# Performance work log

Hardware: AMD Instinct MI355X
Metric: run time of the kernel (lower is better)

## Reference

```python
import jax, jax.numpy as jnp
import numpy as np

N = 50000       # nodes
E = 800000      # edges (avg degree 16)
C_IN = 128
C_OUT = 64
C_HID = 2 * C_OUT  # 128, per Dir_Encoder_GCN


def gcn_conv(x, W, b, src, dst, ew, n):
    """PyG GCNConv: add self-loops (weight 1), symmetric normalization,
    aggregate transformed source features at destination, add bias."""
    loops = jnp.arange(n)
    s = jnp.concatenate([src, loops])                       # [E+N]
    d = jnp.concatenate([dst, loops])                       # [E+N]
    w = jnp.concatenate([ew, jnp.ones((n,), ew.dtype)])     # [E+N]
    deg = jax.ops.segment_sum(w, d, num_segments=n)         # weighted in-degree
    dinv = jnp.where(deg > 0, jax.lax.rsqrt(deg), 0.0)      # deg^{-1/2}
    norm = dinv[s] * w * dinv[d]                            # [E+N]
    xw = x @ W                                              # [n, out]
    out = jax.ops.segment_sum(xw[s] * norm[:, None], d, num_segments=n)
    return out + b


def setup_inputs() -> dict:
    key = jax.random.key(0)
    k1, k2, k3, k4, k5, k6, k7 = jax.random.split(key, 7)
    x = jax.random.normal(k1, (N, C_IN), dtype=jnp.float32)
    edge_index = jax.random.randint(k2, (2, E), 0, N, dtype=jnp.int64)
    edge_weight = jax.random.uniform(k3, (E,), dtype=jnp.float32)
    W1 = jax.random.normal(k4, (C_IN, C_HID), dtype=jnp.float32) * (1.0 / np.sqrt(C_IN))
    b1 = jnp.zeros((C_HID,), dtype=jnp.float32)
    W2 = jax.random.normal(k5, (C_HID, C_OUT), dtype=jnp.float32) * (1.0 / np.sqrt(C_HID))
    b2 = jnp.zeros((C_OUT,), dtype=jnp.float32)
    return {"x": x, "edge_index": edge_index, "edge_weight": edge_weight,
            "W1": W1, "b1": b1, "W2": W2, "b2": b2}


def reference(x, edge_index, edge_weight, W1, b1, W2, b2):
    src, dst = edge_index[0], edge_index[1]
    n = x.shape[0]
    h = jax.nn.elu(gcn_conv(x, W1, b1, src, dst, edge_weight, n))
    return jax.nn.softplus(gcn_conv(h, W2, b2, src, dst, edge_weight, n)) + 1e-4
```

## Files before the change

### kernel.cpp

```cpp
#include <hip/hip_runtime.h>
#include <math.h>

constexpr int CAP    = 48;
constexpr int CAPP   = 49;
constexpr int BIN    = 128;
constexpr int SEGCAP = 2432;
constexpr int CE     = 3136;

typedef short v8s __attribute__((ext_vector_type(8)));
typedef float v4f __attribute__((ext_vector_type(4)));


__device__ __forceinline__ uint f2bf(float f) {
    union { float f; uint i; } v; v.f = f;
    uint r = v.i + 0x7FFFu + ((v.i >> 16) & 1u);
    return r >> 16;
}
__device__ __forceinline__ float bf2f(uint h) {
    union { uint i; float f; } v; v.i = h << 16;
    return v.f;
}
__device__ __forceinline__ void bf8_expand(uint4 q, float* o) {
    uint u[4] = {q.x, q.y, q.z, q.w};
#pragma unroll
    for (int j = 0; j < 4; ++j) {
        union { uint i; float f; } lo, hi;
        lo.i = u[j] << 16;
        hi.i = u[j] & 0xFFFF0000u;
        o[2 * j] = lo.f;
        o[2 * j + 1] = hi.f;
    }
}


template <int COLS>
__device__ __forceinline__ void pack_one(const float* __restrict__ W,
                                         ushort* __restrict__ wpk, int id) {
    constexpr int NT = COLS / 16;
    int lane = id & 63;
    int t = (id >> 6) % NT;
    int c = (id >> 6) / NT;
    int ncol = t * 16 + (lane & 15);
    int k0 = c * 32 + (lane >> 4) * 8;
    ushort hi[8], lo[8];
#pragma unroll
    for (int j = 0; j < 8; ++j) {
        float v = W[(size_t)(k0 + j) * COLS + ncol];
        ushort h = (ushort)f2bf(v);
        hi[j] = h;
        lo[j] = (ushort)f2bf(v - bf2f(h));
    }
    size_t bh = ((size_t)(c * NT + t) * 64 + lane) * 8;
    size_t bl = ((size_t)((4 + c) * NT + t) * 64 + lane) * 8;
    *(uint4*)(wpk + bh) = *(uint4*)hi;
    *(uint4*)(wpk + bl) = *(uint4*)lo;
}

__global__ __launch_bounds__(256) void k_prep(const float* __restrict__ W1,
                                              const float* __restrict__ W2,
                                              ushort* __restrict__ wpk1,
                                              ushort* __restrict__ wpk2,
                                              int* __restrict__ g_bin_cnt) {
    const int blk = blockIdx.x;
    const int tid = threadIdx.x;
    if (blk == 0) {
        g_bin_cnt[tid] = 0;
        g_bin_cnt[tid + 256] = 0;
        return;
    }
    int id = (blk - 1) * 256 + tid;
    if (id < 2048) pack_one<128>(W1, wpk1, id);
    else if (id < 3072) pack_one<64>(W2, wpk2, id - 2048);
}


__global__ __launch_bounds__(256) void k_p1(const int* __restrict__ src,
                                            const int* __restrict__ dst,
                                            const float* __restrict__ ew,
                                            int* __restrict__ g_bin_cnt,
                                            int2* __restrict__ seg, int E) {
    __shared__ int hist[512];
    __shared__ int base[512];
    const int tid = threadIdx.x;
    const int e0 = blockIdx.x * CE;
    const int e1 = min(e0 + CE, E);

    hist[tid] = 0;
    hist[tid + 256] = 0;
    __syncthreads();
    for (int e = e0 + tid; e < e1; e += 256) atomicAdd(&hist[dst[e] >> 7], 1);
    __syncthreads();
    for (int b = tid; b < 512; b += 256)
        base[b] = (hist[b] > 0) ? atomicAdd(&g_bin_cnt[b], hist[b]) : 0;
    __syncthreads();
    hist[tid] = 0;
    hist[tid + 256] = 0;
    __syncthreads();
    for (int e = e0 + tid; e < e1; e += 256) {
        int d = dst[e];
        int b = d >> 7;
        int r = atomicAdd(&hist[b], 1);
        int slot = base[b] + r;
        if (slot < SEGCAP)
            seg[(size_t)b * SEGCAP + slot] =
                make_int2(((d & 127) << 16) | src[e], __float_as_int(ew[e]));
    }
}


__global__ __launch_bounds__(256) void k_p2(const int* __restrict__ g_bin_cnt,
                                            const int2* __restrict__ seg,
                                            int* __restrict__ cnt, float* __restrict__ dinv,
                                            uint* __restrict__ bucket, int N) {
    __shared__ uint lb[BIN * CAPP];
    __shared__ int lcnt[BIN];
    __shared__ float ldeg[BIN];
    const int b = blockIdx.x;
    const int tid = threadIdx.x;
    if (tid < BIN) { lcnt[tid] = 0; ldeg[tid] = 0.f; }
    __syncthreads();

    const int m = min(g_bin_cnt[b], SEGCAP);
    const int2* s = seg + (size_t)b * SEGCAP;
    for (int i = tid; i < m; i += 256) {
        int2 p = s[i];
        int dl = (p.x >> 16) & 127;
        uint sv = (uint)(p.x & 0xFFFF);
        float w = __int_as_float(p.y);
        int slot = atomicAdd(&lcnt[dl], 1);
        if (slot < CAP) lb[dl * CAPP + slot] = sv | (f2bf(w) << 16);
        atomicAdd(&ldeg[dl], w);
    }
    __syncthreads();

    const int node0 = b * BIN;
    if (tid < BIN && node0 + tid < N) {
        cnt[node0 + tid] = min(lcnt[tid], CAP);
        dinv[node0 + tid] = rsqrtf(1.0f + ldeg[tid]);
    }
    const int nn = min(BIN, N - node0);
    for (int i = tid; i < nn * CAP; i += 256) {
        int nl = i / CAP;
        int j = i - nl * CAP;
        if (j < min(lcnt[nl], CAP))
            bucket[((size_t)node0 + nl) * CAP + j] = lb[nl * CAPP + j];
    }
}


__global__ __launch_bounds__(256) void k_gemm1(const float* __restrict__ X,
                                               const ushort* __restrict__ wpk,
                                               const float* __restrict__ dinv,
                                               ushort* __restrict__ Y, int n) {
    constexpr int NT = 8;
    const int wave = threadIdx.x >> 6;
    const int lane = threadIdx.x & 63;
    const int m = lane & 15;
    const int q = lane >> 4;
    const int r0 = blockIdx.x * 64 + wave * 16;

    v4f acc[NT];
#pragma unroll
    for (int t = 0; t < NT; ++t) acc[t] = (v4f){0.f, 0.f, 0.f, 0.f};

    const int arow = min(r0 + m, n - 1);

    for (int c = 0; c < 4; ++c) {
        const float* xp = X + (size_t)arow * 128 + c * 32 + q * 8;
        float4 v0 = *(const float4*)xp;
        float4 v1 = *(const float4*)(xp + 4);
        float f[8] = {v0.x, v0.y, v0.z, v0.w, v1.x, v1.y, v1.z, v1.w};
        union { ushort u[8]; v8s v; } H, L;
#pragma unroll
        for (int j = 0; j < 8; ++j) {
            ushort h = (ushort)f2bf(f[j]);
            H.u[j] = h;
            L.u[j] = (ushort)f2bf(f[j] - bf2f(h));
        }
#pragma unroll
        for (int t = 0; t < NT; ++t) {
            v8s b_hi = *(const v8s*)(wpk + ((size_t)(c * NT + t) * 64 + lane) * 8);
            v8s b_lo = *(const v8s*)(wpk + ((size_t)((4 + c) * NT + t) * 64 + lane) * 8);
            acc[t] = __builtin_amdgcn_mfma_f32_16x16x32_bf16(H.v, b_hi, acc[t], 0, 0, 0);
            acc[t] = __builtin_amdgcn_mfma_f32_16x16x32_bf16(H.v, b_lo, acc[t], 0, 0, 0);
            acc[t] = __builtin_amdgcn_mfma_f32_16x16x32_bf16(L.v, b_hi, acc[t], 0, 0, 0);
        }
    }

#pragma unroll
    for (int r = 0; r < 4; ++r) {
        int row = r0 + q * 4 + r;
        if (row < n) {
            float sc = dinv[row];
#pragma unroll
            for (int t = 0; t < NT; ++t)
                Y[(size_t)row * 128 + t * 16 + m] = (ushort)f2bf(acc[t][r] * sc);
        }
    }
}


template <int C>
__device__ __forceinline__ void gather_accum(const ushort* __restrict__ xw,
                                             const uint* __restrict__ bk, int c,
                                             int laneoff, float* acc) {
    int i = 0;
    for (; i + 8 <= c; i += 8) {
        uint4 e0 = *(const uint4*)(bk + i);
        uint4 e1 = *(const uint4*)(bk + i + 4);
        uint ee[8] = {e0.x, e0.y, e0.z, e0.w, e1.x, e1.y, e1.z, e1.w};
        uint4 q[8];
#pragma unroll
        for (int u = 0; u < 8; ++u)
            q[u] = *(const uint4*)(xw + (size_t)(ee[u] & 0xFFFF) * C + laneoff);
#pragma unroll
        for (int u = 0; u < 8; ++u) {
            float w = bf2f(ee[u] >> 16);
            float f[8];
            bf8_expand(q[u], f);
#pragma unroll
            for (int j = 0; j < 8; ++j) acc[j] += f[j] * w;
        }
    }
    for (; i + 4 <= c; i += 4) {
        uint4 e0 = *(const uint4*)(bk + i);
        uint ee[4] = {e0.x, e0.y, e0.z, e0.w};
        uint4 q[4];
#pragma unroll
        for (int u = 0; u < 4; ++u)
            q[u] = *(const uint4*)(xw + (size_t)(ee[u] & 0xFFFF) * C + laneoff);
#pragma unroll
        for (int u = 0; u < 4; ++u) {
            float w = bf2f(ee[u] >> 16);
            float f[8];
            bf8_expand(q[u], f);
#pragma unroll
            for (int j = 0; j < 8; ++j) acc[j] += f[j] * w;
        }
    }
    for (; i < c; ++i) {
        uint e = bk[i];
        float w = bf2f(e >> 16);
        uint4 qq = *(const uint4*)(xw + (size_t)(e & 0xFFFF) * C + laneoff);
        float f[8];
        bf8_expand(qq, f);
#pragma unroll
        for (int j = 0; j < 8; ++j) acc[j] += f[j] * w;
    }
}


__global__ __launch_bounds__(256) void k_gather_g2(const ushort* __restrict__ xw,
                                                   const float* __restrict__ dinv,
                                                   const float* __restrict__ b1,
                                                   const int* __restrict__ cnt,
                                                   const uint* __restrict__ bucket,
                                                   const ushort* __restrict__ wpk2,
                                                   ushort* __restrict__ hw, int n) {
    constexpr int HS = 136;
    __shared__ ushort hrow[16 * HS];
    __shared__ float sdd[16];
    const int tid = threadIdx.x;
    const int node_l = tid >> 4;
    const int lane16 = tid & 15;
    const int node0 = blockIdx.x * 16;
    const int node = node0 + node_l;
    const bool active = node < n;

    float acc[8] = {0.f, 0.f, 0.f, 0.f, 0.f, 0.f, 0.f, 0.f};
    if (active) {
        {
            float sf[8];
            uint4 q = *(const uint4*)(xw + (size_t)node * 128 + lane16 * 8);
            bf8_expand(q, sf);
#pragma unroll
            for (int j = 0; j < 8; ++j) acc[j] = sf[j];
        }
        int c = min(cnt[node], CAP);
        gather_accum<128>(xw, bucket + (size_t)node * CAP, c, lane16 * 8, acc);

        float dd = dinv[node];
        if (lane16 == 0) sdd[node_l] = dd;
        float4 b0 = *(const float4*)(b1 + lane16 * 8);
        float4 bv = *(const float4*)(b1 + lane16 * 8 + 4);
        float bb[8] = {b0.x, b0.y, b0.z, b0.w, bv.x, bv.y, bv.z, bv.w};
#pragma unroll
        for (int j = 0; j < 8; ++j) {
            float v = bb[j] + dd * acc[j];
            acc[j] = v > 0.f ? v : expm1f(v);
        }
    } else {
        if (lane16 == 0) sdd[node_l] = 0.f;
#pragma unroll
        for (int j = 0; j < 8; ++j) acc[j] = 0.f;
    }

    uint4 o;
    o.x = f2bf(acc[0]) | (f2bf(acc[1]) << 16);
    o.y = f2bf(acc[2]) | (f2bf(acc[3]) << 16);
    o.z = f2bf(acc[4]) | (f2bf(acc[5]) << 16);
    o.w = f2bf(acc[6]) | (f2bf(acc[7]) << 16);
    *(uint4*)(hrow + node_l * HS + lane16 * 8) = o;
    __syncthreads();

    const int wave = tid >> 6;
    const int lane = tid & 63;
    const int mm = lane & 15;
    const int qq = lane >> 4;
    v4f c4 = (v4f){0.f, 0.f, 0.f, 0.f};
    for (int c = 0; c < 4; ++c) {
        v8s a = *(const v8s*)(hrow + mm * HS + c * 32 + qq * 8);
        v8s b_hi = *(const v8s*)(wpk2 + ((size_t)(c * 4 + wave) * 64 + lane) * 8);
        v8s b_lo = *(const v8s*)(wpk2 + ((size_t)((4 + c) * 4 + wave) * 64 + lane) * 8);
        c4 = __builtin_amdgcn_mfma_f32_16x16x32_bf16(a, b_hi, c4, 0, 0, 0);
        c4 = __builtin_amdgcn_mfma_f32_16x16x32_bf16(a, b_lo, c4, 0, 0, 0);
    }
#pragma unroll
    for (int r = 0; r < 4; ++r) {
        int nl = qq * 4 + r;
        int row = node0 + nl;
        if (row < n)
            hw[(size_t)row * 64 + wave * 16 + mm] = (ushort)f2bf(c4[r] * sdd[nl]);
    }
}


__global__ __launch_bounds__(256) void k_gather2(const ushort* __restrict__ hw,
                                                 const float* __restrict__ dinv,
                                                 const float* __restrict__ b2,
                                                 const int* __restrict__ cnt,
                                                 const uint* __restrict__ bucket,
                                                 float* __restrict__ out, int n) {
    constexpr int C = 64, L = 8;
    int node = blockIdx.x * 32 + threadIdx.x / L;
    int lane = threadIdx.x % L;
    if (node >= n) return;

    float acc[8];
    {
        float sf[8];
        uint4 q = *(const uint4*)(hw + (size_t)node * C + lane * 8);
        bf8_expand(q, sf);
#pragma unroll
        for (int j = 0; j < 8; ++j) acc[j] = sf[j];
    }

    int c = min(cnt[node], CAP);
    gather_accum<64>(hw, bucket + (size_t)node * CAP, c, lane * 8, acc);

    float dd = dinv[node];
    float4 b0 = *(const float4*)(b2 + lane * 8);
    float4 bv = *(const float4*)(b2 + lane * 8 + 4);
    float bb[8] = {b0.x, b0.y, b0.z, b0.w, bv.x, bv.y, bv.z, bv.w};
#pragma unroll
    for (int j = 0; j < 8; ++j) {
        float v = bb[j] + dd * acc[j];
        acc[j] = ((v > 20.f) ? v : log1pf(expf(v))) + 1e-4f;
    }
    *(float4*)(out + (size_t)node * C + lane * 8) =
        make_float4(acc[0], acc[1], acc[2], acc[3]);
    *(float4*)(out + (size_t)node * C + lane * 8 + 4) =
        make_float4(acc[4], acc[5], acc[6], acc[7]);
}


extern "C" void kernel_launch(void* const* d_in, const int* in_sizes, int n_in,
                              void* d_out, int out_size, void* d_ws, size_t ws_size,
                              hipStream_t stream) {
    const float* x  = (const float*)d_in[0];
    const int*   ei = (const int*)d_in[1];
    const float* ew = (const float*)d_in[2];
    const float* W1 = (const float*)d_in[3];
    const float* b1 = (const float*)d_in[4];
    const float* W2 = (const float*)d_in[5];
    const float* b2 = (const float*)d_in[6];

    const int N = in_sizes[0] / 128;
    const int E = in_sizes[1] / 2;
    const int* src = ei;
    const int* dst = ei + E;
    float* y = (float*)d_out;

    const int nbins = (N + BIN - 1) / BIN;

    char* p = (char*)d_ws;
    auto take = [&](size_t bytes) {
        char* q = p;
        p += (bytes + 255) & ~(size_t)255;
        return q;
    };

    int*    g_bin_cnt = (int*)take(512 * 4);
    int2*   seg       = (int2*)take((size_t)nbins * SEGCAP * 8);
    int*    cnt       = (int*)take((size_t)N * 4);
    float*  dinv      = (float*)take((size_t)N * 4);
    uint*   bucket    = (uint*)take((size_t)N * CAP * 4);
    ushort* xw        = (ushort*)take((size_t)N * 128 * 2);
    ushort* hw        = (ushort*)take((size_t)N * 64 * 2);
    ushort* wpk1      = (ushort*)take(2 * 4 * 8 * 64 * 8 * 2);
    ushort* wpk2      = (ushort*)take(2 * 4 * 4 * 64 * 8 * 2);

    auto cdiv = [](int a, int b) { return (a + b - 1) / b; };

    k_prep<<<13, 256, 0, stream>>>(W1, W2, wpk1, wpk2, g_bin_cnt);
    k_p1<<<cdiv(E, CE), 256, 0, stream>>>(src, dst, ew, g_bin_cnt, seg, E);
    k_p2<<<nbins, 256, 0, stream>>>(g_bin_cnt, seg, cnt, dinv, bucket, N);

    k_gemm1<<<cdiv(N, 64), 256, 0, stream>>>(x, wpk1, dinv, xw, N);
    k_gather_g2<<<cdiv(N, 16), 256, 0, stream>>>(xw, dinv, b1, cnt, bucket, wpk2, hw, N);
    k_gather2<<<cdiv(N, 32), 256, 0, stream>>>(hw, dinv, b2, cnt, bucket, y, N);
}
```

Before: 192.2 us.

## Co-schedule GEMM1 with edge binning and apply source dinv in gather

Merges the first feature GEMM and the edge-binning pass into one launch whose blocks branch by index, so the compute-bound GEMM can overlap the memory-bound histogram/scatter. To make that possible, the source-side dinv scaling is moved out of the GEMM epilogue and into the gathers, which now load dinv per neighbour. Binning now does a per-block local prefix sum into shared memory with coalesced write-out and per-block offsets, removing the global atomic counter and its zeroing. k_p2 then reads each bin's slice from every block's segment. The costs are an extra scattered dinv load per edge and k_p2 doing 256 short strided reads per bin. k_p2 indexes offsets by thread id, which assumes at most 256 binning blocks (true for this E).

```diff
diff --git a/kernel.cpp b/kernel.cpp
--- a/kernel.cpp
+++ b/kernel.cpp
@@ -1,11 +1,11 @@
 #include <hip/hip_runtime.h>
 #include <math.h>
 
-constexpr int CAP    = 48;
-constexpr int CAPP   = 49;
-constexpr int BIN    = 128;
-constexpr int SEGCAP = 2432;
-constexpr int CE     = 3136;
+constexpr int CAP  = 48;
+constexpr int CAPP = 49;
+constexpr int BIN  = 128;
+constexpr int NB   = 512;
+constexpr int P1E  = 3125;
 
 typedef short v8s __attribute__((ext_vector_type(8)));
 typedef float v4f __attribute__((ext_vector_type(4)));
@@ -59,81 +59,150 @@
 __global__ __launch_bounds__(256) void k_prep(const float* __restrict__ W1,
                                               const float* __restrict__ W2,
                                               ushort* __restrict__ wpk1,
-                                              ushort* __restrict__ wpk2,
-                                              int* __restrict__ g_bin_cnt) {
-    const int blk = blockIdx.x;
-    const int tid = threadIdx.x;
-    if (blk == 0) {
-        g_bin_cnt[tid] = 0;
-        g_bin_cnt[tid + 256] = 0;
-        return;
-    }
-    int id = (blk - 1) * 256 + tid;
+                                              ushort* __restrict__ wpk2) {
+    int id = blockIdx.x * 256 + threadIdx.x;
     if (id < 2048) pack_one<128>(W1, wpk1, id);
     else if (id < 3072) pack_one<64>(W2, wpk2, id - 2048);
 }
 
 
-__global__ __launch_bounds__(256) void k_p1(const int* __restrict__ src,
-                                            const int* __restrict__ dst,
-                                            const float* __restrict__ ew,
-                                            int* __restrict__ g_bin_cnt,
-                                            int2* __restrict__ seg, int E) {
-    __shared__ int hist[512];
-    __shared__ int base[512];
-    const int tid = threadIdx.x;
-    const int e0 = blockIdx.x * CE;
-    const int e1 = min(e0 + CE, E);
-
-    hist[tid] = 0;
-    hist[tid + 256] = 0;
-    __syncthreads();
-    for (int e = e0 + tid; e < e1; e += 256) atomicAdd(&hist[dst[e] >> 7], 1);
-    __syncthreads();
-    for (int b = tid; b < 512; b += 256)
-        base[b] = (hist[b] > 0) ? atomicAdd(&g_bin_cnt[b], hist[b]) : 0;
-    __syncthreads();
-    hist[tid] = 0;
-    hist[tid + 256] = 0;
-    __syncthreads();
-    for (int e = e0 + tid; e < e1; e += 256) {
-        int d = dst[e];
-        int b = d >> 7;
-        int r = atomicAdd(&hist[b], 1);
-        int slot = base[b] + r;
-        if (slot < SEGCAP)
-            seg[(size_t)b * SEGCAP + slot] =
-                make_int2(((d & 127) << 16) | src[e], __float_as_int(ew[e]));
-    }
-}
-
-
-__global__ __launch_bounds__(256) void k_p2(const int* __restrict__ g_bin_cnt,
-                                            const int2* __restrict__ seg,
+__global__ __launch_bounds__(256) void k_mega(const float* __restrict__ X,
+                                              const ushort* __restrict__ wpk1,
+                                              ushort* __restrict__ Y,
+                                              const int* __restrict__ src,
+                                              const int* __restrict__ dst,
+                                              const float* __restrict__ ew,
+                                              int2* __restrict__ seg,
+                                              ushort* __restrict__ g_off,
+                                              int n, int E, int nG1) {
+    if ((int)blockIdx.x < nG1) {
+        constexpr int NT = 8;
+        const int wave = threadIdx.x >> 6;
+        const int lane = threadIdx.x & 63;
+        const int m = lane & 15;
+        const int q = lane >> 4;
+        const int r0 = blockIdx.x * 64 + wave * 16;
+
+        v4f acc[NT];
+#pragma unroll
+        for (int t = 0; t < NT; ++t) acc[t] = (v4f){0.f, 0.f, 0.f, 0.f};
+
+        const int arow = min(r0 + m, n - 1);
+        for (int c = 0; c < 4; ++c) {
+            const float* xp = X + (size_t)arow * 128 + c * 32 + q * 8;
+            float4 v0 = *(const float4*)xp;
+            float4 v1 = *(const float4*)(xp + 4);
+            float f[8] = {v0.x, v0.y, v0.z, v0.w, v1.x, v1.y, v1.z, v1.w};
+            union { ushort u[8]; v8s v; } H, L;
+#pragma unroll
+            for (int j = 0; j < 8; ++j) {
+                ushort h = (ushort)f2bf(f[j]);
+                H.u[j] = h;
+                L.u[j] = (ushort)f2bf(f[j] - bf2f(h));
+            }
+#pragma unroll
+            for (int t = 0; t < NT; ++t) {
+                v8s b_hi = *(const v8s*)(wpk1 + ((size_t)(c * NT + t) * 64 + lane) * 8);
+                v8s b_lo = *(const v8s*)(wpk1 + ((size_t)((4 + c) * NT + t) * 64 + lane) * 8);
+                acc[t] = __builtin_amdgcn_mfma_f32_16x16x32_bf16(H.v, b_hi, acc[t], 0, 0, 0);
+                acc[t] = __builtin_amdgcn_mfma_f32_16x16x32_bf16(H.v, b_lo, acc[t], 0, 0, 0);
+                acc[t] = __builtin_amdgcn_mfma_f32_16x16x32_bf16(L.v, b_hi, acc[t], 0, 0, 0);
+            }
+        }
+#pragma unroll
+        for (int r = 0; r < 4; ++r) {
+            int row = r0 + q * 4 + r;
+            if (row < n) {
+#pragma unroll
+                for (int t = 0; t < NT; ++t)
+                    Y[(size_t)row * 128 + t * 16 + m] = (ushort)f2bf(acc[t][r]);
+            }
+        }
+    } else {
+        __shared__ int2 stg[P1E];
+        __shared__ int hist[NB];
+        __shared__ int base_[NB];
+        __shared__ int wsum[4];
+        const int b = blockIdx.x - nG1;
+        const int tid = threadIdx.x;
+        const int e0 = b * P1E;
+        const int e1 = min(e0 + P1E, E);
+        const int m = e1 - e0;
+
+        hist[tid] = 0;
+        hist[tid + 256] = 0;
+        __syncthreads();
+        for (int e = e0 + tid; e < e1; e += 256) atomicAdd(&hist[dst[e] >> 7], 1);
+        __syncthreads();
+        {
+            int v0 = hist[2 * tid], v1 = hist[2 * tid + 1];
+            int v = v0 + v1;
+            int x = v;
+            int lane = tid & 63, wid = tid >> 6;
+#pragma unroll
+            for (int off = 1; off < 64; off <<= 1) {
+                int t = __shfl_up(x, off, 64);
+                if (lane >= off) x += t;
+            }
+            if (lane == 63) wsum[wid] = x;
+            __syncthreads();
+            int woff = 0;
+#pragma unroll
+            for (int w = 0; w < 4; ++w) woff += (w < wid) ? wsum[w] : 0;
+            int excl = x - v + woff;
+            base_[2 * tid] = excl;
+            base_[2 * tid + 1] = excl + v0;
+        }
+        __syncthreads();
+        hist[tid] = base_[tid];
+        hist[tid + 256] = base_[tid + 256];
+        __syncthreads();
+        for (int e = e0 + tid; e < e1; e += 256) {
+            int d = dst[e];
+            int bin = d >> 7;
+            int pos = atomicAdd(&hist[bin], 1);
+            stg[pos] = make_int2(((d & 127) << 16) | src[e], __float_as_int(ew[e]));
+        }
+        __syncthreads();
+        int2* so = seg + (size_t)b * P1E;
+        for (int i = tid; i < m; i += 256) so[i] = stg[i];
+        ushort* go = g_off + (size_t)b * 513;
+        for (int i = tid; i < NB; i += 256) go[i] = (ushort)base_[i];
+        if (tid == 0) go[512] = (ushort)m;
+    }
+}
+
+
+__global__ __launch_bounds__(256) void k_p2(const int2* __restrict__ seg,
+                                            const ushort* __restrict__ g_off,
                                             int* __restrict__ cnt, float* __restrict__ dinv,
                                             uint* __restrict__ bucket, int N) {
     __shared__ uint lb[BIN * CAPP];
     __shared__ int lcnt[BIN];
     __shared__ float ldeg[BIN];
-    const int b = blockIdx.x;
+    const int bin = blockIdx.x;
     const int tid = threadIdx.x;
     if (tid < BIN) { lcnt[tid] = 0; ldeg[tid] = 0.f; }
     __syncthreads();
 
-    const int m = min(g_bin_cnt[b], SEGCAP);
-    const int2* s = seg + (size_t)b * SEGCAP;
-    for (int i = tid; i < m; i += 256) {
-        int2 p = s[i];
-        int dl = (p.x >> 16) & 127;
-        uint sv = (uint)(p.x & 0xFFFF);
-        float w = __int_as_float(p.y);
-        int slot = atomicAdd(&lcnt[dl], 1);
-        if (slot < CAP) lb[dl * CAPP + slot] = sv | (f2bf(w) << 16);
-        atomicAdd(&ldeg[dl], w);
+    {
+        const ushort* go = g_off + (size_t)tid * 513;
+        int off = go[bin];
+        int end = go[bin + 1];
+        const int2* sp = seg + (size_t)tid * P1E;
+        for (int j = off; j < end; ++j) {
+            int2 p = sp[j];
+            int dl = (p.x >> 16) & 127;
+            uint sv = (uint)(p.x & 0xFFFF);
+            float w = __int_as_float(p.y);
+            int slot = atomicAdd(&lcnt[dl], 1);
+            if (slot < CAP) lb[dl * CAPP + slot] = sv | (f2bf(w) << 16);
+            atomicAdd(&ldeg[dl], w);
+        }
     }
     __syncthreads();
 
-    const int node0 = b * BIN;
+    const int node0 = bin * BIN;
     if (tid < BIN && node0 + tid < N) {
         cnt[node0 + tid] = min(lcnt[tid], CAP);
         dinv[node0 + tid] = rsqrtf(1.0f + ldeg[tid]);
@@ -148,60 +217,9 @@
 }
 
 
-__global__ __launch_bounds__(256) void k_gemm1(const float* __restrict__ X,
-                                               const ushort* __restrict__ wpk,
-                                               const float* __restrict__ dinv,
-                                               ushort* __restrict__ Y, int n) {
-    constexpr int NT = 8;
-    const int wave = threadIdx.x >> 6;
-    const int lane = threadIdx.x & 63;
-    const int m = lane & 15;
-    const int q = lane >> 4;
-    const int r0 = blockIdx.x * 64 + wave * 16;
-
-    v4f acc[NT];
-#pragma unroll
-    for (int t = 0; t < NT; ++t) acc[t] = (v4f){0.f, 0.f, 0.f, 0.f};
-
-    const int arow = min(r0 + m, n - 1);
-
-    for (int c = 0; c < 4; ++c) {
-        const float* xp = X + (size_t)arow * 128 + c * 32 + q * 8;
-        float4 v0 = *(const float4*)xp;
-        float4 v1 = *(const float4*)(xp + 4);
-        float f[8] = {v0.x, v0.y, v0.z, v0.w, v1.x, v1.y, v1.z, v1.w};
-        union { ushort u[8]; v8s v; } H, L;
-#pragma unroll
-        for (int j = 0; j < 8; ++j) {
-            ushort h = (ushort)f2bf(f[j]);
-            H.u[j] = h;
-            L.u[j] = (ushort)f2bf(f[j] - bf2f(h));
-        }
-#pragma unroll
-        for (int t = 0; t < NT; ++t) {
-            v8s b_hi = *(const v8s*)(wpk + ((size_t)(c * NT + t) * 64 + lane) * 8);
-            v8s b_lo = *(const v8s*)(wpk + ((size_t)((4 + c) * NT + t) * 64 + lane) * 8);
-            acc[t] = __builtin_amdgcn_mfma_f32_16x16x32_bf16(H.v, b_hi, acc[t], 0, 0, 0);
-            acc[t] = __builtin_amdgcn_mfma_f32_16x16x32_bf16(H.v, b_lo, acc[t], 0, 0, 0);
-            acc[t] = __builtin_amdgcn_mfma_f32_16x16x32_bf16(L.v, b_hi, acc[t], 0, 0, 0);
-        }
-    }
-
-#pragma unroll
-    for (int r = 0; r < 4; ++r) {
-        int row = r0 + q * 4 + r;
-        if (row < n) {
-            float sc = dinv[row];
-#pragma unroll
-            for (int t = 0; t < NT; ++t)
-                Y[(size_t)row * 128 + t * 16 + m] = (ushort)f2bf(acc[t][r] * sc);
-        }
-    }
-}
-
-
 template <int C>
 __device__ __forceinline__ void gather_accum(const ushort* __restrict__ xw,
+                                             const float* __restrict__ dinv,
                                              const uint* __restrict__ bk, int c,
                                              int laneoff, float* acc) {
     int i = 0;
@@ -210,12 +228,16 @@
         uint4 e1 = *(const uint4*)(bk + i + 4);
         uint ee[8] = {e0.x, e0.y, e0.z, e0.w, e1.x, e1.y, e1.z, e1.w};
         uint4 q[8];
-#pragma unroll
-        for (int u = 0; u < 8; ++u)
-            q[u] = *(const uint4*)(xw + (size_t)(ee[u] & 0xFFFF) * C + laneoff);
+        float dv[8];
 #pragma unroll
         for (int u = 0; u < 8; ++u) {
-            float w = bf2f(ee[u] >> 16);
+            uint s = ee[u] & 0xFFFF;
+            q[u] = *(const uint4*)(xw + (size_t)s * C + laneoff);
+            dv[u] = dinv[s];
+        }
+#pragma unroll
+        for (int u = 0; u < 8; ++u) {
+            float w = dv[u] * bf2f(ee[u] >> 16);
             float f[8];
             bf8_expand(q[u], f);
 #pragma unroll
@@ -226,12 +248,16 @@
         uint4 e0 = *(const uint4*)(bk + i);
         uint ee[4] = {e0.x, e0.y, e0.z, e0.w};
         uint4 q[4];
-#pragma unroll
-        for (int u = 0; u < 4; ++u)
-            q[u] = *(const uint4*)(xw + (size_t)(ee[u] & 0xFFFF) * C + laneoff);
+        float dv[4];
 #pragma unroll
         for (int u = 0; u < 4; ++u) {
-            float w = bf2f(ee[u] >> 16);
+            uint s = ee[u] & 0xFFFF;
+            q[u] = *(const uint4*)(xw + (size_t)s * C + laneoff);
+            dv[u] = dinv[s];
+        }
+#pragma unroll
+        for (int u = 0; u < 4; ++u) {
+            float w = dv[u] * bf2f(ee[u] >> 16);
             float f[8];
             bf8_expand(q[u], f);
 #pragma unroll
@@ -240,8 +266,9 @@
     }
     for (; i < c; ++i) {
         uint e = bk[i];
-        float w = bf2f(e >> 16);
-        uint4 qq = *(const uint4*)(xw + (size_t)(e & 0xFFFF) * C + laneoff);
+        uint s = e & 0xFFFF;
+        float w = dinv[s] * bf2f(e >> 16);
+        uint4 qq = *(const uint4*)(xw + (size_t)s * C + laneoff);
         float f[8];
         bf8_expand(qq, f);
 #pragma unroll
@@ -259,7 +286,6 @@
                                                    ushort* __restrict__ hw, int n) {
     constexpr int HS = 136;
     __shared__ ushort hrow[16 * HS];
-    __shared__ float sdd[16];
     const int tid = threadIdx.x;
     const int node_l = tid >> 4;
     const int lane16 = tid & 15;
@@ -269,18 +295,17 @@
 
     float acc[8] = {0.f, 0.f, 0.f, 0.f, 0.f, 0.f, 0.f, 0.f};
     if (active) {
+        float dd = dinv[node];
         {
             float sf[8];
             uint4 q = *(const uint4*)(xw + (size_t)node * 128 + lane16 * 8);
             bf8_expand(q, sf);
 #pragma unroll
-            for (int j = 0; j < 8; ++j) acc[j] = sf[j];
+            for (int j = 0; j < 8; ++j) acc[j] = sf[j] * dd;
         }
         int c = min(cnt[node], CAP);
-        gather_accum<128>(xw, bucket + (size_t)node * CAP, c, lane16 * 8, acc);
-
-        float dd = dinv[node];
-        if (lane16 == 0) sdd[node_l] = dd;
+        gather_accum<128>(xw, dinv, bucket + (size_t)node * CAP, c, lane16 * 8, acc);
+
         float4 b0 = *(const float4*)(b1 + lane16 * 8);
         float4 bv = *(const float4*)(b1 + lane16 * 8 + 4);
         float bb[8] = {b0.x, b0.y, b0.z, b0.w, bv.x, bv.y, bv.z, bv.w};
@@ -289,10 +314,6 @@
             float v = bb[j] + dd * acc[j];
             acc[j] = v > 0.f ? v : expm1f(v);
         }
-    } else {
-        if (lane16 == 0) sdd[node_l] = 0.f;
-#pragma unroll
-        for (int j = 0; j < 8; ++j) acc[j] = 0.f;
     }
 
     uint4 o;
@@ -317,10 +338,9 @@
     }
 #pragma unroll
     for (int r = 0; r < 4; ++r) {
-        int nl = qq * 4 + r;
-        int row = node0 + nl;
+        int row = node0 + qq * 4 + r;
         if (row < n)
-            hw[(size_t)row * 64 + wave * 16 + mm] = (ushort)f2bf(c4[r] * sdd[nl]);
+            hw[(size_t)row * 64 + wave * 16 + mm] = (ushort)f2bf(c4[r]);
     }
 }
 
@@ -336,19 +356,19 @@
     int lane = threadIdx.x % L;
     if (node >= n) return;
 
+    float dd = dinv[node];
     float acc[8];
     {
         float sf[8];
         uint4 q = *(const uint4*)(hw + (size_t)node * C + lane * 8);
         bf8_expand(q, sf);
 #pragma unroll
-        for (int j = 0; j < 8; ++j) acc[j] = sf[j];
+        for (int j = 0; j < 8; ++j) acc[j] = sf[j] * dd;
     }
 
     int c = min(cnt[node], CAP);
-    gather_accum<64>(hw, bucket + (size_t)node * CAP, c, lane * 8, acc);
-
-    float dd = dinv[node];
+    gather_accum<64>(hw, dinv, bucket + (size_t)node * CAP, c, lane * 8, acc);
+
     float4 b0 = *(const float4*)(b2 + lane * 8);
     float4 bv = *(const float4*)(b2 + lane * 8 + 4);
     float bb[8] = {b0.x, b0.y, b0.z, b0.w, bv.x, bv.y, bv.z, bv.w};
@@ -381,7 +401,10 @@
     const int* dst = ei + E;
     float* y = (float*)d_out;
 
-    const int nbins = (N + BIN - 1) / BIN;
+    auto cdiv = [](int a, int b) { return (a + b - 1) / b; };
+    const int nbins = cdiv(N, BIN);
+    const int nG1   = cdiv(N, 64);
+    const int nP1   = cdiv(E, P1E);
 
     char* p = (char*)d_ws;
     auto take = [&](size_t bytes) {
@@ -390,23 +413,19 @@
         return q;
     };
 
-    int*    g_bin_cnt = (int*)take(512 * 4);
-    int2*   seg       = (int2*)take((size_t)nbins * SEGCAP * 8);
-    int*    cnt       = (int*)take((size_t)N * 4);
-    float*  dinv      = (float*)take((size_t)N * 4);
-    uint*   bucket    = (uint*)take((size_t)N * CAP * 4);
-    ushort* xw        = (ushort*)take((size_t)N * 128 * 2);
-    ushort* hw        = (ushort*)take((size_t)N * 64 * 2);
-    ushort* wpk1      = (ushort*)take(2 * 4 * 8 * 64 * 8 * 2);
-    ushort* wpk2      = (ushort*)take(2 * 4 * 4 * 64 * 8 * 2);
-
-    auto cdiv = [](int a, int b) { return (a + b - 1) / b; };
-
-    k_prep<<<13, 256, 0, stream>>>(W1, W2, wpk1, wpk2, g_bin_cnt);
-    k_p1<<<cdiv(E, CE), 256, 0, stream>>>(src, dst, ew, g_bin_cnt, seg, E);
-    k_p2<<<nbins, 256, 0, stream>>>(g_bin_cnt, seg, cnt, dinv, bucket, N);
-
-    k_gemm1<<<cdiv(N, 64), 256, 0, stream>>>(x, wpk1, dinv, xw, N);
+    int2*   seg    = (int2*)take((size_t)nP1 * P1E * 8);
+    ushort* g_off  = (ushort*)take((size_t)nP1 * 513 * 2);
+    int*    cnt    = (int*)take((size_t)N * 4);
+    float*  dinv   = (float*)take((size_t)N * 4);
+    uint*   bucket = (uint*)take((size_t)N * CAP * 4);
+    ushort* xw     = (ushort*)take((size_t)N * 128 * 2);
+    ushort* hw     = (ushort*)take((size_t)N * 64 * 2);
+    ushort* wpk1   = (ushort*)take(2 * 4 * 8 * 64 * 8 * 2);
+    ushort* wpk2   = (ushort*)take(2 * 4 * 4 * 64 * 8 * 2);
+
+    k_prep<<<12, 256, 0, stream>>>(W1, W2, wpk1, wpk2);
+    k_mega<<<nG1 + nP1, 256, 0, stream>>>(x, wpk1, xw, src, dst, ew, seg, g_off, N, E, nG1);
+    k_p2<<<nbins, 256, 0, stream>>>(seg, g_off, cnt, dinv, bucket, N);
     k_gather_g2<<<cdiv(N, 16), 256, 0, stream>>>(xw, dinv, b1, cnt, bucket, wpk2, hw, N);
     k_gather2<<<cdiv(N, 32), 256, 0, stream>>>(hw, dinv, b2, cnt, bucket, y, N);
 }
```

After: 181.8 us, median of 2. 1.06x faster.
